# Optimization experiments

Hardware: AMD Instinct MI355X
Metric: run time of the kernel (lower is better)

Reference implementation:

```python
import jax, jax.numpy as jnp
import numpy as np

SLOPE = 25.0  # snntorch surrogate.fast_sigmoid default slope
NUM_STEPS = 15

@jax.custom_vjp
def spike(x):
    # Heaviside forward, fast-sigmoid surrogate backward
    return (x > 0).astype(x.dtype)

def _spike_fwd(x):
    return spike(x), x

def _spike_bwd(x, g):
    return (g / (SLOPE * jnp.abs(x) + 1.0) ** 2,)

spike.defvjp(_spike_fwd, _spike_bwd)


def setup_inputs() -> dict:
    p, hidden, B = 97, 512, 32768
    key = jax.random.key(0)
    ks = jax.random.split(key, 6)
    s1 = 1.0 / np.sqrt(2 * hidden)
    s2 = 1.0 / np.sqrt(hidden)
    return {
        "x": jax.random.randint(ks[0], (B, 2), 0, p, dtype=jnp.int64 if jax.config.jax_enable_x64 else jnp.int32),
        "embed_w": jax.random.normal(ks[1], (p, hidden), jnp.float32),
        "W1": jax.random.uniform(ks[2], (hidden, 2 * hidden), jnp.float32, -s1, s1),
        "b1": jax.random.uniform(ks[3], (hidden,), jnp.float32, -s1, s1),
        "W2": jax.random.uniform(ks[4], (p, hidden), jnp.float32, -s2, s2),
        "b2": jax.random.uniform(ks[5], (p,), jnp.float32, -s2, s2),
        "beta1": jnp.float32(0.85),
        "beta2": jnp.float32(0.85),
        "thr1": jnp.float32(1.0),
        "thr2": jnp.float32(1.0),
    }


def reference(x, embed_w, W1, b1, W2, b2, beta1, beta2, thr1, thr2):
    # parameter clamps (done in-place under no_grad in torch)
    beta1 = jnp.clip(beta1, 0.1, 0.9)
    beta2 = jnp.clip(beta2, 0.1, 0.9)
    thr1 = jnp.maximum(thr1, 0.1)
    thr2 = jnp.maximum(thr2, 0.1)

    B = x.shape[0]
    hidden = embed_w.shape[1]
    p = W2.shape[0]

    emb = embed_w[x].reshape(B, 2 * hidden)          # [B, 2H]
    cur1 = emb @ W1.T + b1                           # constant across steps [B, H]

    def step(carry, _):
        mem1, mem2 = carry
        # lif1: Leaky, reset_mechanism='subtract'; reset computed from prev mem (detached)
        reset = jax.lax.stop_gradient((mem1 - thr1 > 0).astype(mem1.dtype))
        mem1 = jnp.clip(beta1, 0.0, 1.0) * mem1 + cur1 - reset * thr1
        spk1 = spike(mem1 - thr1)                    # [B, H]
        cur2 = spk1 @ W2.T + b2                      # [B, p]
        # lif2: reset_mechanism='none'
        mem2 = jnp.clip(beta2, 0.0, 1.0) * mem2 + cur2
        return (mem1, mem2), None

    mem1 = jnp.zeros((B, hidden), cur1.dtype)
    mem2 = jnp.zeros((B, p), cur1.dtype)
    (mem1, mem2), _ = jax.lax.scan(step, (mem1, mem2), None, length=NUM_STEPS)
    return mem2  # final membrane potential of output layer
```

## Files before the change

### kernel.cpp

```cpp
#include <hip/hip_runtime.h>
#include <cstddef>

#define PMOD 97
#define HID 512
#define NPAIR 9409
#define NSTEPS 15

typedef __attribute__((ext_vector_type(8))) short short8;
typedef __attribute__((ext_vector_type(4))) short short4_t;
typedef __attribute__((ext_vector_type(4))) float f32x4;

static __device__ __forceinline__ unsigned short f2bf_rn(float f) {
    unsigned u = __float_as_uint(f);
    u += 0x7FFFu + ((u >> 16) & 1u);
    return (unsigned short)(u >> 16);
}
static __device__ __forceinline__ float bf2f(unsigned short h) {
    return __uint_as_float(((unsigned)h) << 16);
}
static __device__ __forceinline__ void split_hilo(const float* __restrict__ p,
                                                  short8& hi, short8& lo) {
    const float4 v0 = *(const float4*)p;
    const float4 v1 = *(const float4*)(p + 4);
    const float vv[8] = {v0.x, v0.y, v0.z, v0.w, v1.x, v1.y, v1.z, v1.w};
#pragma unroll
    for (int q = 0; q < 8; ++q) {
        const unsigned short hb = f2bf_rn(vv[q]);
        hi[q] = (short)hb;
        lo[q] = (short)f2bf_rn(vv[q] - bf2f(hb));
    }
}

__global__ __launch_bounds__(256) void k_abm(const float* __restrict__ embed,
                                             const float* __restrict__ W1,
                                             const float* __restrict__ W2,
                                             const float* __restrict__ b1,
                                             short* __restrict__ w2bf,
                                             float* __restrict__ Ap,
                                             float* __restrict__ Bm) {
    __shared__ f32x4 red[3][64];

    const int t = threadIdx.x;
    const int lane = t & 63;
    const int kq = t >> 6;

    const int gid = blockIdx.x * 256 + t;
    if (gid < PMOD * HID / 4) {
        const float4 v = ((const float4*)W2)[gid];
        const float vv[4] = {v.x, v.y, v.z, v.w};
        short4_t h4;
#pragma unroll
        for (int q = 0; q < 4; ++q) h4[q] = (short)f2bf_rn(vv[q]);
        *(short4_t*)(w2bf + gid * 4) = h4;
    }

    const int mt = blockIdx.x >> 6;
    const int ng = blockIdx.x & 63;
    int e = mt * 16 + (lane & 15);
    if (e > PMOD - 1) e = PMOD - 1;
    const int n = ng * 16 + (lane & 15);
    const int h = n & 511;
    const int half = n >> 9;
    const int kbase = kq * 128 + (lane >> 4) * 8;

    f32x4 acc = (f32x4){0.f, 0.f, 0.f, 0.f};
#pragma unroll
    for (int kt = 0; kt < 4; ++kt) {
        const int k = kbase + kt * 32;
        short8 ahi, alo, bhi, blo;
        split_hilo(embed + (size_t)e * HID + k, ahi, alo);
        split_hilo(W1 + (size_t)h * 1024 + half * HID + k, bhi, blo);
        acc = __builtin_amdgcn_mfma_f32_16x16x32_bf16(ahi, bhi, acc, 0, 0, 0);
        acc = __builtin_amdgcn_mfma_f32_16x16x32_bf16(alo, bhi, acc, 0, 0, 0);
        acc = __builtin_amdgcn_mfma_f32_16x16x32_bf16(ahi, blo, acc, 0, 0, 0);
    }

    if (kq != 0) red[kq - 1][lane] = acc;
    __syncthreads();
    if (kq == 0) {
        acc += red[0][lane];
        acc += red[1][lane];
        acc += red[2][lane];
        const float bias = half ? 0.f : b1[h];
#pragma unroll
        for (int reg = 0; reg < 4; ++reg) {
            const int er = mt * 16 + (lane >> 4) * 4 + reg;
            if (er < PMOD) {
                if (half == 0) Ap[(size_t)er * HID + h] = acc[reg] + bias;
                else           Bm[(size_t)er * HID + h] = acc[reg];
            }
        }
    }
}

__global__ __launch_bounds__(512) void k_pairs(const float* __restrict__ Ap,
                                               const float* __restrict__ Bm,
                                               const short* __restrict__ w2bf,
                                               const float* __restrict__ b2,
                                               const float* __restrict__ pbeta1,
                                               const float* __restrict__ pbeta2,
                                               const float* __restrict__ pthr1,
                                               float* __restrict__ pairOut) {
    __shared__ short8 wfrag[16][64];
    __shared__ f32x4 red[2][3][4][64];

    const float beta1 = fminf(fmaxf(pbeta1[0], 0.1f), 0.9f);
    const float beta2 = fminf(fmaxf(pbeta2[0], 0.1f), 0.9f);
    const float thr   = fmaxf(pthr1[0], 0.1f);

    const int t = threadIdx.x;
    const int lane = t & 63;
    const int w = t >> 6;
    const int pblk = blockIdx.x * 16;

    const int pid0 = pblk + (lane & 15);
    const int pid  = (pid0 < NPAIR) ? pid0 : (NPAIR - 1);
    const unsigned i = (unsigned)pid / PMOD;
    const unsigned j = (unsigned)pid - i * PMOD;

#pragma unroll
    for (int kk = 0; kk < 2; ++kk) {
        const int kt = 2 * w + kk;
        const int h = kt * 32 + (lane >> 4) * 8;
        const float* ap = Ap + (size_t)i * HID + h;
        const float* bp = Bm + (size_t)j * HID + h;
        const float4 a0 = *(const float4*)ap;
        const float4 a1 = *(const float4*)(ap + 4);
        const float4 g0 = *(const float4*)bp;
        const float4 g1 = *(const float4*)(bp + 4);
        float c[8] = {a0.x + g0.x, a0.y + g0.y, a0.z + g0.z, a0.w + g0.w,
                      a1.x + g1.x, a1.y + g1.y, a1.z + g1.z, a1.w + g1.w};
        float cm[8], m[8], wv[8];
        bool sb[8];
#pragma unroll
        for (int q = 0; q < 8; ++q) {
            cm[q] = c[q] - thr; m[q] = 0.f; wv[q] = 0.f; sb[q] = false;
        }
        for (int s = 0; s < NSTEPS; ++s) {
#pragma unroll
            for (int q = 0; q < 8; ++q) {
                const float cadj = sb[q] ? cm[q] : c[q];
                m[q] = fmaf(beta1, m[q], cadj);
                sb[q] = m[q] > thr;
                wv[q] = fmaf(beta2, wv[q], sb[q] ? 1.f : 0.f);
            }
        }
        short8 af;
#pragma unroll
        for (int q = 0; q < 8; ++q) af[q] = (short)f2bf_rn(wv[q]);
        wfrag[kt][lane] = af;
    }
    __syncthreads();

    const int kq = w & 3;
    const int nh = w >> 2;
    const int ntb = nh * 4;

    f32x4 acc[4];
#pragma unroll
    for (int q = 0; q < 4; ++q) acc[q] = (f32x4){0.f, 0.f, 0.f, 0.f};

#pragma unroll
    for (int kk = 0; kk < 4; ++kk) {
        const int kt = kq * 4 + kk;
        const short8 af = wfrag[kt][lane];
        const int k = kt * 32 + (lane >> 4) * 8;
#pragma unroll
        for (int q = 0; q < 4; ++q) {
            const int nt = ntb + q;
            if (nt < 7) {
                const int o0 = nt * 16 + (lane & 15);
                const int oc = (o0 < PMOD) ? o0 : (PMOD - 1);
                const short8 bf = *(const short8*)(w2bf + (size_t)oc * HID + k);
                acc[q] = __builtin_amdgcn_mfma_f32_16x16x32_bf16(af, bf, acc[q], 0, 0, 0);
            }
        }
    }

    if (kq != 0) {
#pragma unroll
        for (int q = 0; q < 4; ++q)
            if (ntb + q < 7) red[nh][kq - 1][q][lane] = acc[q];
    }
    __syncthreads();
    if (kq == 0) {
        float S = 0.f;
#pragma unroll
        for (int s = 0; s < NSTEPS; ++s) S = fmaf(beta2, S, 1.f);
#pragma unroll
        for (int q = 0; q < 4; ++q) {
            const int nt = ntb + q;
            if (nt < 7) {
                f32x4 a = acc[q];
                a += red[nh][0][q][lane];
                a += red[nh][1][q][lane];
                a += red[nh][2][q][lane];
                const int o = nt * 16 + (lane & 15);
                if (o < PMOD) {
                    const float bias = b2[o] * S;
#pragma unroll
                    for (int reg = 0; reg < 4; ++reg) {
                        const int prow = pblk + (lane >> 4) * 4 + reg;
                        if (prow < NPAIR)
                            pairOut[(size_t)prow * PMOD + o] = a[reg] + bias;
                    }
                }
            }
        }
    }
}

__global__ __launch_bounds__(256) void k_scatter(const int* __restrict__ x,
                                                 const float* __restrict__ pairOut,
                                                 float* __restrict__ out,
                                                 int total) {
    const unsigned idx = blockIdx.x * 256u + threadIdx.x;
    if (idx >= (unsigned)total) return;
    const unsigned b = idx / PMOD;
    const unsigned o = idx - b * PMOD;
    const int pid = x[2 * b] * PMOD + x[2 * b + 1];
    out[idx] = pairOut[(size_t)pid * PMOD + o];
}

extern "C" void kernel_launch(void* const* d_in, const int* in_sizes, int n_in,
                              void* d_out, int out_size, void* d_ws, size_t ws_size,
                              hipStream_t stream) {
    const int*   x     = (const int*)d_in[0];
    const float* embed = (const float*)d_in[1];
    const float* W1    = (const float*)d_in[2];
    const float* b1    = (const float*)d_in[3];
    const float* W2    = (const float*)d_in[4];
    const float* b2    = (const float*)d_in[5];
    const float* beta1 = (const float*)d_in[6];
    const float* beta2 = (const float*)d_in[7];
    const float* thr1  = (const float*)d_in[8];

    float* out = (float*)d_out;
    const int B = in_sizes[0] / 2;

    char* ws = (char*)d_ws;
    float* pairOut = (float*)(ws);
    short* w2bf    = (short*)(ws + 3650816);
    float* Ap      = (float*)(ws + 3750144);
    float* Bm      = (float*)(ws + 3948800);

    k_abm<<<448, 256, 0, stream>>>(embed, W1, W2, b1, w2bf, Ap, Bm);

    const int nblk = (NPAIR + 15) / 16;
    k_pairs<<<nblk, 512, 0, stream>>>(Ap, Bm, w2bf, b2, beta1, beta2, thr1, pairOut);

    const int total = B * PMOD;
    k_scatter<<<(total + 255) / 256, 256, 0, stream>>>(x, pairOut, out, total);
}
```

Baseline: 46.27 us.

## Fuse output scatter into pair kernel using per-pair batch index buckets

k_abm now also buckets batch indices by (x0, x1) pair, using atomic counters into a fixed-capacity list. k_pairs then writes each pair's computed output row straight to every batch row that uses it. This removes the pairOut intermediate buffer and the separate scatter kernel, so the intermediate write/read round trip and one launch go away. In exchange it adds a memset, atomics, and serialized scattered writes in the reduction waves. Pairs with more than CAP occurrences would not be handled correctly, because the loop bound is not clamped to CAP.

```diff
diff --git a/kernel.cpp b/kernel.cpp
--- a/kernel.cpp
+++ b/kernel.cpp
@@ -5,6 +5,7 @@
 #define HID 512
 #define NPAIR 9409
 #define NSTEPS 15
+#define CAP 96
 
 typedef __attribute__((ext_vector_type(8))) short short8;
 typedef __attribute__((ext_vector_type(4))) short short4_t;
@@ -35,7 +36,11 @@
                                              const float* __restrict__ W1,
                                              const float* __restrict__ W2,
                                              const float* __restrict__ b1,
+                                             const int* __restrict__ x,
+                                             int nB,
                                              short* __restrict__ w2bf,
+                                             int* __restrict__ cnt,
+                                             int* __restrict__ blist,
                                              float* __restrict__ Ap,
                                              float* __restrict__ Bm) {
     __shared__ f32x4 red[3][64];
@@ -43,8 +48,8 @@
     const int t = threadIdx.x;
     const int lane = t & 63;
     const int kq = t >> 6;
-
     const int gid = blockIdx.x * 256 + t;
+
     if (gid < PMOD * HID / 4) {
         const float4 v = ((const float4*)W2)[gid];
         const float vv[4] = {v.x, v.y, v.z, v.w};
@@ -52,6 +57,14 @@
 #pragma unroll
         for (int q = 0; q < 4; ++q) h4[q] = (short)f2bf_rn(vv[q]);
         *(short4_t*)(w2bf + gid * 4) = h4;
+    }
+
+    if (gid < nB) {
+        const int x0 = x[2 * gid];
+        const int x1 = x[2 * gid + 1];
+        const int pid = x0 * PMOD + x1;
+        const int slot = atomicAdd(&cnt[pid], 1);
+        if (slot < CAP) blist[pid * CAP + slot] = gid;
     }
 
     const int mt = blockIdx.x >> 6;
@@ -100,7 +113,9 @@
                                                const float* __restrict__ pbeta1,
                                                const float* __restrict__ pbeta2,
                                                const float* __restrict__ pthr1,
-                                               float* __restrict__ pairOut) {
+                                               const int* __restrict__ cnt,
+                                               const int* __restrict__ blist,
+                                               float* __restrict__ out) {
     __shared__ short8 wfrag[16][64];
     __shared__ f32x4 red[2][3][4][64];
 
@@ -187,39 +202,38 @@
         float S = 0.f;
 #pragma unroll
         for (int s = 0; s < NSTEPS; ++s) S = fmaf(beta2, S, 1.f);
+
+        float biasq[4];
 #pragma unroll
         for (int q = 0; q < 4; ++q) {
             const int nt = ntb + q;
             if (nt < 7) {
-                f32x4 a = acc[q];
-                a += red[nh][0][q][lane];
-                a += red[nh][1][q][lane];
-                a += red[nh][2][q][lane];
+                acc[q] += red[nh][0][q][lane];
+                acc[q] += red[nh][1][q][lane];
+                acc[q] += red[nh][2][q][lane];
                 const int o = nt * 16 + (lane & 15);
-                if (o < PMOD) {
-                    const float bias = b2[o] * S;
-#pragma unroll
-                    for (int reg = 0; reg < 4; ++reg) {
-                        const int prow = pblk + (lane >> 4) * 4 + reg;
-                        if (prow < NPAIR)
-                            pairOut[(size_t)prow * PMOD + o] = a[reg] + bias;
+                biasq[q] = (o < PMOD) ? b2[o] * S : 0.f;
+            } else biasq[q] = 0.f;
+        }
+
+#pragma unroll
+        for (int reg = 0; reg < 4; ++reg) {
+            const int prow = pblk + (lane >> 4) * 4 + reg;
+            const int nb = (prow < NPAIR) ? cnt[prow] : 0;
+            for (int s = 0; s < nb; ++s) {
+                const int b = blist[prow * CAP + s];
+                float* orow = out + (size_t)b * PMOD;
+#pragma unroll
+                for (int q = 0; q < 4; ++q) {
+                    const int nt = ntb + q;
+                    if (nt < 7) {
+                        const int o = nt * 16 + (lane & 15);
+                        if (o < PMOD) orow[o] = acc[q][reg] + biasq[q];
                     }
                 }
             }
         }
     }
-}
-
-__global__ __launch_bounds__(256) void k_scatter(const int* __restrict__ x,
-                                                 const float* __restrict__ pairOut,
-                                                 float* __restrict__ out,
-                                                 int total) {
-    const unsigned idx = blockIdx.x * 256u + threadIdx.x;
-    if (idx >= (unsigned)total) return;
-    const unsigned b = idx / PMOD;
-    const unsigned o = idx - b * PMOD;
-    const int pid = x[2 * b] * PMOD + x[2 * b + 1];
-    out[idx] = pairOut[(size_t)pid * PMOD + o];
 }
 
 extern "C" void kernel_launch(void* const* d_in, const int* in_sizes, int n_in,
@@ -239,16 +253,17 @@
     const int B = in_sizes[0] / 2;
 
     char* ws = (char*)d_ws;
-    float* pairOut = (float*)(ws);
-    short* w2bf    = (short*)(ws + 3650816);
-    float* Ap      = (float*)(ws + 3750144);
-    float* Bm      = (float*)(ws + 3948800);
-
-    k_abm<<<448, 256, 0, stream>>>(embed, W1, W2, b1, w2bf, Ap, Bm);
+    int*   cnt   = (int*)(ws);
+    int*   blist = (int*)(ws + 40960);
+    short* w2bf  = (short*)(ws + 3654016);
+    float* Ap    = (float*)(ws + 3753344);
+    float* Bm    = (float*)(ws + 3952000);
+
+    hipMemsetAsync(cnt, 0, NPAIR * sizeof(int), stream);
+
+    k_abm<<<448, 256, 0, stream>>>(embed, W1, W2, b1, x, B, w2bf, cnt, blist, Ap, Bm);
 
     const int nblk = (NPAIR + 15) / 16;
-    k_pairs<<<nblk, 512, 0, stream>>>(Ap, Bm, w2bf, b2, beta1, beta2, thr1, pairOut);
-
-    const int total = B * PMOD;
-    k_scatter<<<(total + 255) / 256, 256, 0, stream>>>(x, pairOut, out, total);
-}
+    k_pairs<<<nblk, 512, 0, stream>>>(Ap, Bm, w2bf, b2, beta1, beta2, thr1,
+                                      cnt, blist, out);
+}
```

Result: slower. 54.25 us (+17.2%).
